# Kernel optimization log

Measured on AMD Instinct MI355X. Metric: run time of the kernel, lower is better.

The kernel has to match this reference:

```python
import jax, jax.numpy as jnp
import numpy as np

# ---- config constants (from configs) ----
B, L, C = 32, 512, 16
DM, DS, DCONV, EXP, EL = 128, 16, 4, 2, 2
PATCH, STRIDE, PAD, PRED = 16, 8, 8, 96
DIN = EXP * DM            # 256
DTR = (DM + 15) // 16     # dt_rank = 8
NPATCH = (L + 2 * PAD - PATCH) // STRIDE + 1   # 65
HNF = DM * NPATCH         # 8320
EPS = 1e-5


def setup_inputs() -> dict:
    key = jax.random.key(0)
    ks = jax.random.split(key, 14)
    n = jax.random.normal
    A_log = jnp.tile(jnp.log(jnp.arange(1, DS + 1, dtype=jnp.float32)), (EL, DIN, 1))
    return {
        "x_enc": n(ks[0], (B, L, C), jnp.float32),
        "x_mark_enc": n(ks[1], (B, L, 4), jnp.float32),
        "pe_w": n(ks[2], (DM, 1, PATCH), jnp.float32) * (1.0 / np.sqrt(PATCH)),
        "pe_b": n(ks[3], (DM,), jnp.float32) * 0.02,
        "in_proj_w": n(ks[4], (EL, 2 * DIN, DM), jnp.float32) * (1.0 / np.sqrt(DM)),
        "conv_w": n(ks[5], (EL, DIN, DCONV), jnp.float32) * (1.0 / np.sqrt(DCONV)),
        "conv_b": n(ks[6], (EL, DIN), jnp.float32) * 0.02,
        "x_proj_w": n(ks[7], (EL, DTR + 2 * DS, DIN), jnp.float32) * (1.0 / np.sqrt(DIN)),
        "dt_proj_w": n(ks[8], (EL, DIN, DTR), jnp.float32) * (1.0 / np.sqrt(DTR)),
        "dt_proj_b": n(ks[9], (EL, DIN), jnp.float32) * 0.1,
        "A_log": A_log,
        "D": jnp.ones((EL, DIN), jnp.float32),
        "out_proj_w": n(ks[10], (EL, DM, DIN), jnp.float32) * (1.0 / np.sqrt(DIN)),
        "head_w": n(ks[11], (PRED, HNF), jnp.float32) * (1.0 / np.sqrt(HNF)),
    }


def _silu(x):
    return x * jax.nn.sigmoid(x)


def _mamba(x, in_w, cw, cb, xp_w, dtp_w, dtp_b, A_log, Dp, out_w):
    # x: (b, P, DM)
    b = x.shape[0]
    xz = jnp.einsum('bpd,ed->bpe', x, in_w)            # (b, P, 2*DIN)
    xin, z = jnp.split(xz, 2, axis=-1)
    # causal depthwise conv1d over time
    xt = xin.transpose(0, 2, 1)                        # (b, DIN, P)
    conv = jax.lax.conv_general_dilated(
        xt, cw[:, None, :], (1,), [(DCONV - 1, 0)],
        dimension_numbers=('NCH', 'OIH', 'NCH'), feature_group_count=DIN)
    xc = _silu((conv + cb[None, :, None]).transpose(0, 2, 1))   # (b, P, DIN)
    dbc = jnp.einsum('bpd,ed->bpe', xc, xp_w)          # (b, P, DTR+2*DS)
    dt, Bm, Cm = jnp.split(dbc, [DTR, DTR + DS], axis=-1)
    dt = jax.nn.softplus(jnp.einsum('bpr,dr->bpd', dt, dtp_w) + dtp_b)  # (b,P,DIN)
    A = -jnp.exp(A_log)                                # (DIN, DS)

    def step(h, inp):
        dt_t, B_t, C_t, x_t = inp                      # (b,DIN),(b,DS),(b,DS),(b,DIN)
        dA = jnp.exp(dt_t[:, :, None] * A)             # (b,DIN,DS)
        h = dA * h + (dt_t * x_t)[:, :, None] * B_t[:, None, :]
        y = jnp.einsum('bds,bs->bd', h, C_t)
        return h, y

    h0 = jnp.zeros((b, DIN, DS), x.dtype)
    xs = (dt.transpose(1, 0, 2), Bm.transpose(1, 0, 2),
          Cm.transpose(1, 0, 2), xc.transpose(1, 0, 2))
    _, ys = jax.lax.scan(step, h0, xs)                 # (P, b, DIN)
    y = ys.transpose(1, 0, 2) + xc * Dp
    y = y * _silu(z)
    return jnp.einsum('bpd,od->bpo', y, out_w)         # (b, P, DM)


def reference(x_enc, x_mark_enc, pe_w, pe_b, in_proj_w, conv_w, conv_b,
              x_proj_w, dt_proj_w, dt_proj_b, A_log, D, out_proj_w, head_w):
    # RevIN-style normalization (stats detached, as in torch)
    mean = jax.lax.stop_gradient(jnp.mean(x_enc, axis=1, keepdims=True))
    xc = x_enc - mean
    std = jax.lax.stop_gradient(jnp.sqrt(jnp.var(xc, axis=1, keepdims=True) + EPS))
    xn = xc / std                                      # (B, L, C)
    x = xn.transpose(0, 2, 1).reshape(B * C, 1, L)
    # patch embedding conv
    p = jax.lax.conv_general_dilated(
        x, pe_w, (STRIDE,), [(PAD, PAD)],
        dimension_numbers=('NCH', 'OIH', 'NCH')) + pe_b[None, :, None]
    p = p.transpose(0, 2, 1)                           # (B*C, NPATCH, DM)
    for i in range(EL):
        p = _mamba(p, in_proj_w[i], conv_w[i], conv_b[i], x_proj_w[i],
                   dt_proj_w[i], dt_proj_b[i], A_log[i], D[i], out_proj_w[i])
    flat = p.reshape(B * C, HNF)
    head = flat @ head_w.T                             # (B*C, PRED)
    out = head.reshape(B, C, PRED).transpose(0, 2, 1)  # (B, PRED, C)
    return out * std + mean
```

## Files before the change

### kernel.cpp

```cpp
#include <hip/hip_runtime.h>

typedef __attribute__((ext_vector_type(8))) short bf16x8;
typedef __attribute__((ext_vector_type(8))) unsigned short u16x8;
typedef __attribute__((ext_vector_type(4))) float f32x4;

#define DEV static __device__ __forceinline__

constexpr int DM   = 128;
constexpr int DIN  = 256;
constexpr int NP   = 65;
constexpr int NSEQ = 512;
constexpr int HNF  = 8320;
constexpr int LOPL = NSEQ*HNF;

constexpr size_t OFF_FLAG = 0;
constexpr size_t OFF_MEAN = 16;
constexpr size_t OFF_STD  = OFF_MEAN + 512;
constexpr size_t OFF_ANEG = OFF_STD  + 512;
constexpr size_t OFF_CONVW= OFF_ANEG + 8192;
constexpr size_t OFF_CONVB= OFF_CONVW+ 2048;
constexpr size_t OFF_DTPB = OFF_CONVB+ 512;
constexpr size_t OFF_DD   = OFF_DTPB + 512;
constexpr size_t OFF_PEWT = OFF_DD   + 512;
constexpr size_t OFF_PEB  = OFF_PEWT + 2048;
constexpr size_t OFF_INF  = OFF_PEB  + 128;
constexpr size_t OFF_XPF  = OFF_INF  + 65536;
constexpr size_t OFF_OPF  = OFF_XPF  + 12288;
constexpr size_t OFF_HDF  = OFF_OPF  + 32768;
constexpr size_t OFF_PA   = OFF_HDF  + 399360;
constexpr size_t OFF_PB   = OFF_PA   + (size_t)NSEQ*HNF;
constexpr size_t OFF_HACC = OFF_PB;

DEV float b2f(unsigned short u){ union{unsigned v; float f;} x; x.v = ((unsigned)u)<<16; return x.f; }
DEV unsigned short f2b(float f){
  union{float f32; unsigned u;} x; x.f32 = f;
  unsigned r = x.u + 0x7fffu + ((x.u>>16)&1u);
  return (unsigned short)(r>>16);
}
DEV void split2(float v, unsigned short& h, unsigned short& l){
  h = f2b(v); l = f2b(v - b2f(h));
}
DEV float load_in(const void* p, size_t i, int isbf){
  return isbf ? b2f(((const unsigned short*)p)[i]) : ((const float*)p)[i];
}
DEV f32x4 mfma16(bf16x8 a, bf16x8 b, f32x4 c){
  return __builtin_amdgcn_mfma_f32_16x16x32_bf16(a,b,c,0,0,0);
}
constexpr float LOG2E = 1.4426950408889634f;
constexpr float LN2   = 0.6931471805599453f;
DEV float ex2(float x){ float r; asm("v_exp_f32 %0, %1" : "=v"(r) : "v"(x)); return r; }
DEV float lg2(float x){ float r; asm("v_log_f32 %0, %1" : "=v"(r) : "v"(x)); return r; }
DEV float frcp(float x){ float r; asm("v_rcp_f32 %0, %1" : "=v"(r) : "v"(x)); return r; }
DEV float sigm(float x){ return frcp(1.f + ex2(-x*LOG2E)); }
DEV float softplus(float x){
  float t = ex2(-fabsf(x)*LOG2E);
  return fmaxf(x,0.f) + LN2*lg2(1.f + t);
}
DEV int detect_bf16_wave(const void* x, int tid){
  const unsigned short* u = (const unsigned short*)x;
  unsigned short v = u[2*tid];
  int e = (v>>7)&0xff;
  int pred = (v==0) || (e>=100 && e<=141);
  unsigned long long m = __ballot(pred);
  return __popcll(m) >= 48;
}
DEV u16x8 load8_cvt(const void* p, size_t off, int isbf){
  u16x8 o;
  if (isbf){
    o = *(const u16x8*)((const unsigned short*)p + off);
  } else {
    const float* s = (const float*)p + off;
    float4 a = *(const float4*)(s), b = *(const float4*)(s+4);
    o[0]=f2b(a.x); o[1]=f2b(a.y); o[2]=f2b(a.z); o[3]=f2b(a.w);
    o[4]=f2b(b.x); o[5]=f2b(b.y); o[6]=f2b(b.z); o[7]=f2b(b.w);
  }
  return o;
}

constexpr size_t N_SMALL = 13952;
constexpr size_t N_IN8 = 16384, N_XP8 = 3072, N_OP8 = 8192, N_HD8 = 99840;
constexpr size_t N_BIG8 = N_IN8+N_XP8+N_OP8+N_HD8;
constexpr int NPREP = (int)((N_SMALL + N_BIG8 + 255)/256);
__global__ void k_pre(const void* x_enc, const void* pe_w, const void* pe_b,
                      const void* in_w, const void* conv_w, const void* conv_b,
                      const void* xp_w, const void* dtp_b,
                      const void* A_log, const void* Dm, const void* op_w,
                      const void* head_w, float* __restrict__ ws)
{
  const int tid = threadIdx.x;
  __shared__ int sflag;
  __shared__ float sx[512];
  __shared__ float spe[16*128];
  __shared__ float spb[128];
  __shared__ float rs[8], rq[8], sm[2];

  if (tid < 64){
    int f = detect_bf16_wave(x_enc, tid);
    if (tid==0) sflag = f;
  }
  __syncthreads();
  const int isbf = sflag;

  if (blockIdx.x < NPREP){
    if (blockIdx.x==0 && tid==0) ws[OFF_FLAG] = (float)isbf;
    size_t i = (size_t)blockIdx.x*256 + tid;
    const size_t nA=8192, nCW=2048, nCB=512, nDB=512, nD=512, nPW=2048, nPB=128;
    if (i < N_SMALL){
      if (i < nA){ ws[OFF_ANEG+i] = -__expf(load_in(A_log,i,isbf)); return; } i -= nA;
      if (i < nCW){ ws[OFF_CONVW+i] = load_in(conv_w,i,isbf); return; } i -= nCW;
      if (i < nCB){ ws[OFF_CONVB+i] = load_in(conv_b,i,isbf); return; } i -= nCB;
      if (i < nDB){ ws[OFF_DTPB+i]  = load_in(dtp_b,i,isbf); return; } i -= nDB;
      if (i < nD){  ws[OFF_DD+i]    = load_in(Dm,i,isbf); return; } i -= nD;
      if (i < nPW){ size_t k=i>>7, dm=i&127; ws[OFF_PEWT+i]=load_in(pe_w, dm*16+k, isbf); return; } i -= nPW;
      ws[OFF_PEB+i] = load_in(pe_b,i,isbf); return;
    }
    size_t i8 = i - N_SMALL;
    if (i8 >= N_BIG8) return;
    if (i8 < N_IN8){
      size_t lane=i8&63, kk=(i8>>6)&3, nt=(i8>>8)&31, l=i8>>13;
      size_t e=nt*16+(lane&15), k0=kk*32+((lane>>4)*8);
      ((u16x8*)((unsigned short*)(ws+OFF_INF)))[i8] =
        load8_cvt(in_w, (l*512+e)*128 + k0, isbf);
      return;
    } i8 -= N_IN8;
    if (i8 < N_XP8){
      size_t lane=i8&63, kk=(i8>>6)&7; size_t rest=i8>>9;
      size_t nt=rest%3, l=rest/3;
      size_t o=nt*16+(lane&15), k0=kk*32+((lane>>4)*8);
      u16x8 v;
      if (o<40) v = load8_cvt(xp_w, (l*40+o)*256 + k0, isbf);
      else { u16x8 z = {0,0,0,0,0,0,0,0}; v = z; }
      ((u16x8*)((unsigned short*)(ws+OFF_XPF)))[i8] = v;
      return;
    } i8 -= N_XP8;
    if (i8 < N_OP8){
      size_t lane=i8&63, kk=(i8>>6)&7, nt=(i8>>9)&7, l=i8>>12;
      size_t dm=nt*16+(lane&15), k0=kk*32+((lane>>4)*8);
      ((u16x8*)((unsigned short*)(ws+OFF_OPF)))[i8] =
        load8_cvt(op_w, (l*128+dm)*256 + k0, isbf);
      return;
    } i8 -= N_OP8;
    {
      size_t lane=i8&63, t=i8>>6;
      size_t kk=t%260, nt=t/260;
      size_t pr=nt*16+(lane&15), k0=kk*32+((lane>>4)*8);
      ((u16x8*)((unsigned short*)(ws+OFF_HDF)))[i8] =
        load8_cvt(head_w, pr*8320 + k0, isbf);
      return;
    }
  }

  const int n = blockIdx.x - NPREP;
  const int b = n>>4, c = n&15;

  float v0 = load_in(x_enc, ((size_t)b*512+tid)*16 + c, isbf);
  float v1 = load_in(x_enc, ((size_t)b*512+tid+256)*16 + c, isbf);
  float s = v0+v1, q = v0*v0+v1*v1;
  for (int o=32;o;o>>=1){ s += __shfl_down(s,o,64); q += __shfl_down(q,o,64); }
  const int w = tid>>6, lane = tid&63;
  if (lane==0){ rs[w]=s; rq[w]=q; }
  __syncthreads();
  if (tid==0){
    float S=rs[0]+rs[1]+rs[2]+rs[3], Q=rq[0]+rq[1]+rq[2]+rq[3];
    float mean = S*(1.f/512.f);
    float var = fmaxf(Q*(1.f/512.f)-mean*mean, 0.f);
    float sd = sqrtf(var+1e-5f);
    sm[0]=mean; sm[1]=1.f/sd;
    ws[OFF_MEAN+n]=mean; ws[OFF_STD+n]=sd;
  }
  __syncthreads();
  const float mean=sm[0], rstd=sm[1];
  sx[tid]=(v0-mean)*rstd; sx[tid+256]=(v1-mean)*rstd;
  for (int i=tid;i<2048;i+=256) spe[i]=load_in(pe_w, (size_t)(i&127)*16 + (i>>7), isbf);
  if (tid<128) spb[tid]=load_in(pe_b, tid, isbf);
  __syncthreads();

  unsigned short* pa_hi = (unsigned short*)(ws+OFF_PA);
  unsigned short* pa_lo = pa_hi + LOPL;
  for (int i=tid;i<NP*DM;i+=256){
    int t=i>>7, dm=i&127;
    float acc = spb[dm];
    int j0 = t*8-8;
    #pragma unroll
    for (int k=0;k<16;k++){ int j=j0+k; if ((unsigned)j<512u) acc += sx[j]*spe[k*128+dm]; }
    unsigned short h,lo2; split2(acc,h,lo2);
    pa_hi[(size_t)n*HNF+i] = h;
    pa_lo[(size_t)n*HNF+i] = lo2;
  }
}

__global__ __launch_bounds__(256,2)
void k_layer(int l, const unsigned short* __restrict__ pin,
             unsigned short* __restrict__ pout, float* __restrict__ ws,
             const void* __restrict__ dtp_w_raw)
{
  const int n = blockIdx.x, tid = threadIdx.x;
  const int w = tid>>6, lane = tid&63, ml = lane&15, quad = lane>>4;
  const int isbf = ws[OFF_FLAG] != 0.f;

  __shared__ __align__(16) unsigned char arena[79040];
  unsigned short* s_hi = (unsigned short*)arena;
  unsigned short* s_lo = (unsigned short*)(arena+34320);
  float* s_dbc = (float*)(arena+68640);

  const unsigned short* INF = (const unsigned short*)(ws+OFF_INF) + (size_t)l*65536;
  const unsigned short* XPF = (const unsigned short*)(ws+OFF_XPF) + (size_t)l*12288;
  const unsigned short* OPF = (const unsigned short*)(ws+OFF_OPF) + (size_t)l*32768;
  const unsigned short* phi = pin + (size_t)n*HNF;
  const unsigned short* plo = phi + LOPL;

  for (int pass=0; pass<2; ++pass){
    f32x4 acc[5][2];
    #pragma unroll
    for (int mt=0;mt<5;mt++){
      #pragma unroll
      for (int p2=0;p2<2;p2++){ f32x4 z={0.f,0.f,0.f,0.f}; acc[mt][p2]=z; }
    }
    bf16x8 ah[2][5], al[2][5];
    #pragma unroll
    for (int mt=0;mt<5;mt++){
      int row = mt*16+ml; if (row>64) row=64;
      ah[0][mt] = *(const bf16x8*)&phi[(size_t)row*128 + quad*8];
      al[0][mt] = *(const bf16x8*)&plo[(size_t)row*128 + quad*8];
    }
    #pragma unroll
    for (int kk=0;kk<4;kk++){
      const int cur = kk&1, nxt = cur^1;
      bf16x8 b0 = *(const bf16x8*)&INF[((size_t)((pass*8+w*2+0)*4+kk))*512 + lane*8];
      bf16x8 b1 = *(const bf16x8*)&INF[((size_t)((pass*8+w*2+1)*4+kk))*512 + lane*8];
      if (kk<3){
        #pragma unroll
        for (int mt=0;mt<5;mt++){
          int row = mt*16+ml; if (row>64) row=64;
          ah[nxt][mt] = *(const bf16x8*)&phi[(size_t)row*128 + (kk+1)*32 + quad*8];
          al[nxt][mt] = *(const bf16x8*)&plo[(size_t)row*128 + (kk+1)*32 + quad*8];
        }
      }
      #pragma unroll
      for (int mt=0;mt<5;mt++)
        acc[mt][0] = mfma16(ah[cur][mt],b0,mfma16(al[cur][mt],b0,acc[mt][0]));
      #pragma unroll
      for (int mt=0;mt<5;mt++)
        acc[mt][1] = mfma16(ah[cur][mt],b1,mfma16(al[cur][mt],b1,acc[mt][1]));
    }
    #pragma unroll
    for (int p2=0;p2<2;p2++){
      int e = (pass*8 + w*2 + p2)*16 + ml;
      #pragma unroll
      for (int mt=0;mt<5;mt++){
        #pragma unroll
        for (int r=0;r<4;r++){
          int t = mt*16+quad*4+r;
          if (t<NP){
            unsigned short h,lo2; split2(acc[mt][p2][r],h,lo2);
            s_hi[t*264+e]=h; s_lo[t*264+e]=lo2;
          }
        }
      }
    }
  }
  __syncthreads();

  {
    const int d = tid;
    const float4 wv = ((const float4*)(ws+OFF_CONVW))[l*256+d];
    const float bb = ws[OFF_CONVB + l*256+d];
    float x0=0.f,x1=0.f,x2=0.f;
    int t = 0;
    for (; t+4<=NP; t+=4){
      float xi0 = b2f(s_hi[(t+0)*264+d]) + b2f(s_lo[(t+0)*264+d]);
      float xi1 = b2f(s_hi[(t+1)*264+d]) + b2f(s_lo[(t+1)*264+d]);
      float xi2 = b2f(s_hi[(t+2)*264+d]) + b2f(s_lo[(t+2)*264+d]);
      float xi3 = b2f(s_hi[(t+3)*264+d]) + b2f(s_lo[(t+3)*264+d]);
      float v0 = bb + wv.x*x0  + wv.y*x1  + wv.z*x2  + wv.w*xi0;
      float v1 = bb + wv.x*x1  + wv.y*x2  + wv.z*xi0 + wv.w*xi1;
      float v2 = bb + wv.x*x2  + wv.y*xi0 + wv.z*xi1 + wv.w*xi2;
      float v3 = bb + wv.x*xi0 + wv.y*xi1 + wv.z*xi2 + wv.w*xi3;
      x0=xi1; x1=xi2; x2=xi3;
      float s0 = v0*sigm(v0), s1 = v1*sigm(v1), s2 = v2*sigm(v2), s3 = v3*sigm(v3);
      unsigned short h,lo2;
      split2(s0,h,lo2); s_hi[(t+0)*264+d]=h; s_lo[(t+0)*264+d]=lo2;
      split2(s1,h,lo2); s_hi[(t+1)*264+d]=h; s_lo[(t+1)*264+d]=lo2;
      split2(s2,h,lo2); s_hi[(t+2)*264+d]=h; s_lo[(t+2)*264+d]=lo2;
      split2(s3,h,lo2); s_hi[(t+3)*264+d]=h; s_lo[(t+3)*264+d]=lo2;
    }
    for (; t<NP; ++t){
      float xi = b2f(s_hi[t*264+d]) + b2f(s_lo[t*264+d]);
      float v = bb + wv.x*x0 + wv.y*x1 + wv.z*x2 + wv.w*xi;
      x0=x1; x1=x2; x2=xi;
      float sv = v * sigm(v);
      unsigned short h,lo2; split2(sv,h,lo2);
      s_hi[t*264+d]=h; s_lo[t*264+d]=lo2;
    }
  }
  __syncthreads();

  for (int tile=w; tile<15; tile+=4){
    int mt=tile/3, nt=tile%3;
    f32x4 acc={0.f,0.f,0.f,0.f};
    #pragma unroll
    for (int kk=0;kk<8;kk++){
      int row = mt*16+ml; if (row>64) row=64;
      bf16x8 ah = *(const bf16x8*)&s_hi[row*264 + kk*32 + quad*8];
      bf16x8 al = *(const bf16x8*)&s_lo[row*264 + kk*32 + quad*8];
      bf16x8 b  = *(const bf16x8*)&XPF[((size_t)(nt*8+kk))*512 + lane*8];
      acc = mfma16(ah,b,mfma16(al,b,acc));
    }
    int o = nt*16+ml;
    #pragma unroll
    for (int r=0;r<4;r++){
      int t=mt*16+quad*4+r;
      if (t<NP && o<40) s_dbc[t*40+o] = acc[r];
    }
  }
  __syncthreads();

  {
    const int d = tid;
    float A2[16];
    {
      const float4* ap = (const float4*)(ws+OFF_ANEG) + ((size_t)l*256+d)*4;
      #pragma unroll
      for (int qq=0;qq<4;qq++){
        float4 t4 = ap[qq];
        A2[qq*4]=t4.x*LOG2E; A2[qq*4+1]=t4.y*LOG2E; A2[qq*4+2]=t4.z*LOG2E; A2[qq*4+3]=t4.w*LOG2E;
      }
    }
    int fastbit = 1;
    #pragma unroll
    for (int ss=0;ss<16;ss++){
      float ex = -(float)(ss+1)*LOG2E;
      fastbit &= (fabsf(A2[ss]-ex) <= 1e-4f*(float)(ss+1)) ? 1 : 0;
    }
    const int fastu = __all(fastbit);
    const float Dv = ws[OFF_DD + l*256+d];
    const float bias = ws[OFF_DTPB + l*256+d];
    float wdt[8];
    #pragma unroll
    for (int r=0;r<8;r++) wdt[r] = load_in(dtp_w_raw, ((size_t)l*256+d)*8+r, isbf);
    float h[16];
    #pragma unroll
    for (int ss=0;ss<16;ss++) h[ss]=0.f;

    float4 q0 = *(const float4*)&s_dbc[0];
    float4 q1 = *(const float4*)&s_dbc[4];
    float xh = b2f(s_hi[d]), xl = b2f(s_lo[d]);

    for (int t=0;t<NP;t++){
      const float* row = &s_dbc[t*40];
      float xv = xh + xl;
      float4 b0=*(const float4*)(row+8),  b1=*(const float4*)(row+12),
             b2v=*(const float4*)(row+16), b3=*(const float4*)(row+20);
      float4 c0=*(const float4*)(row+24), c1=*(const float4*)(row+28),
             c2=*(const float4*)(row+32), c3=*(const float4*)(row+36);
      float4 nq0, nq1; float nxh=0.f, nxl=0.f;
      if (t+1<NP){
        const float* nrow = &s_dbc[(t+1)*40];
        nq0 = *(const float4*)(nrow);
        nq1 = *(const float4*)(nrow+4);
        nxh = b2f(s_hi[(t+1)*264+d]); nxl = b2f(s_lo[(t+1)*264+d]);
      }
      float p0 = q0.x*wdt[0] + q0.y*wdt[1];
      float p1 = q0.z*wdt[2] + q0.w*wdt[3];
      float p2 = q1.x*wdt[4] + q1.y*wdt[5];
      float p3 = q1.z*wdt[6] + q1.w*wdt[7];
      float din = (bias + p0 + p1) + (p2 + p3);
      float dtv = softplus(din);
      float dtx = dtv*xv;
      float Bv[16], Cv[16];
      Bv[0]=b0.x;Bv[1]=b0.y;Bv[2]=b0.z;Bv[3]=b0.w; Bv[4]=b1.x;Bv[5]=b1.y;Bv[6]=b1.z;Bv[7]=b1.w;
      Bv[8]=b2v.x;Bv[9]=b2v.y;Bv[10]=b2v.z;Bv[11]=b2v.w; Bv[12]=b3.x;Bv[13]=b3.y;Bv[14]=b3.z;Bv[15]=b3.w;
      Cv[0]=c0.x;Cv[1]=c0.y;Cv[2]=c0.z;Cv[3]=c0.w; Cv[4]=c1.x;Cv[5]=c1.y;Cv[6]=c1.z;Cv[7]=c1.w;
      Cv[8]=c2.x;Cv[9]=c2.y;Cv[10]=c2.z;Cv[11]=c2.w; Cv[12]=c3.x;Cv[13]=c3.y;Cv[14]=c3.z;Cv[15]=c3.w;
      float rr[16];
      if (fastu){
        float r1 = ex2(-dtv*LOG2E);
        float r2=r1*r1;
        float r3=r2*r1, r4=r2*r2;
        float r5=r4*r1, r6=r4*r2, r7=r4*r3, r8=r4*r4;
        rr[0]=r1; rr[1]=r2; rr[2]=r3; rr[3]=r4;
        rr[4]=r5; rr[5]=r6; rr[6]=r7; rr[7]=r8;
        rr[8]=r8*r1; rr[9]=r8*r2; rr[10]=r8*r3; rr[11]=r8*r4;
        rr[12]=r8*r5; rr[13]=r8*r6; rr[14]=r8*r7; rr[15]=r8*r8;
      } else {
        #pragma unroll
        for (int ss=0;ss<16;ss++) rr[ss] = ex2(dtv*A2[ss]);
      }
      float y0 = 0.f, y1 = 0.f;
      #pragma unroll
      for (int ss=0;ss<16;ss+=2){
        h[ss]   = rr[ss]*h[ss]     + dtx*Bv[ss];
        h[ss+1] = rr[ss+1]*h[ss+1] + dtx*Bv[ss+1];
        y0 += h[ss]*Cv[ss];
        y1 += h[ss+1]*Cv[ss+1];
      }
      float g0 = (y0+y1) + xv*Dv;
      unsigned short hh,lo2; split2(g0,hh,lo2);
      s_hi[t*264+d]=hh; s_lo[t*264+d]=lo2;
      q0=nq0; q1=nq1; xh=nxh; xl=nxl;
    }
  }
  __syncthreads();

  {
    bf16x8 ah[2][4], al[2][4];
    {
      int row = ml;
      #pragma unroll
      for (int kk=0;kk<4;kk++){
        ah[0][kk] = *(const bf16x8*)&phi[(size_t)row*128 + kk*32 + quad*8];
        al[0][kk] = *(const bf16x8*)&plo[(size_t)row*128 + kk*32 + quad*8];
      }
    }
    #pragma unroll
    for (int mt=0; mt<5; ++mt){
      const int cur = mt&1, nxt = cur^1;
      if (mt<4){
        int row = (mt+1)*16+ml; if (row>64) row=64;
        #pragma unroll
        for (int kk=0;kk<4;kk++){
          ah[nxt][kk] = *(const bf16x8*)&phi[(size_t)row*128 + kk*32 + quad*8];
          al[nxt][kk] = *(const bf16x8*)&plo[(size_t)row*128 + kk*32 + quad*8];
        }
      }
      #pragma unroll
      for (int j=0;j<4;j++){
        int nt = w + j*4;
        f32x4 acc={0.f,0.f,0.f,0.f};
        #pragma unroll
        for (int kk=0;kk<4;kk++){
          bf16x8 b = *(const bf16x8*)&INF[((size_t)((16+nt)*4+kk))*512 + lane*8];
          acc = mfma16(ah[cur][kk],b,mfma16(al[cur][kk],b,acc));
        }
        int d = nt*16+ml;
        #pragma unroll
        for (int r=0;r<4;r++){
          int t = mt*16+quad*4+r;
          if (t<NP){
            float g0 = b2f(s_hi[t*264+d]) + b2f(s_lo[t*264+d]);
            float zv = acc[r];
            float g = g0 * zv * sigm(zv);
            unsigned short hh,lo2; split2(g,hh,lo2);
            s_hi[t*264+d]=hh; s_lo[t*264+d]=lo2;
          }
        }
      }
    }
  }
  __syncthreads();

  {
    f32x4 acc[5][2];
    #pragma unroll
    for (int mt=0;mt<5;mt++){
      #pragma unroll
      for (int p2=0;p2<2;p2++){ f32x4 z={0.f,0.f,0.f,0.f}; acc[mt][p2]=z; }
    }
    bf16x8 bpre[2][2];
    bpre[0][0] = *(const bf16x8*)&OPF[((size_t)((w*2+0)*8+0))*512 + lane*8];
    bpre[0][1] = *(const bf16x8*)&OPF[((size_t)((w*2+1)*8+0))*512 + lane*8];
    #pragma unroll
    for (int kk=0;kk<8;kk++){
      const int cur = kk&1, nxt = cur^1;
      if (kk<7){
        bpre[nxt][0] = *(const bf16x8*)&OPF[((size_t)((w*2+0)*8+kk+1))*512 + lane*8];
        bpre[nxt][1] = *(const bf16x8*)&OPF[((size_t)((w*2+1)*8+kk+1))*512 + lane*8];
      }
      bf16x8 ah[5], al[5];
      #pragma unroll
      for (int mt=0;mt<5;mt++){
        int row = mt*16+ml; if (row>64) row=64;
        ah[mt] = *(const bf16x8*)&s_hi[row*264 + kk*32 + quad*8];
        al[mt] = *(const bf16x8*)&s_lo[row*264 + kk*32 + quad*8];
      }
      #pragma unroll
      for (int mt=0;mt<5;mt++)
        acc[mt][0] = mfma16(ah[mt],bpre[cur][0],mfma16(al[mt],bpre[cur][0],acc[mt][0]));
      #pragma unroll
      for (int mt=0;mt<5;mt++)
        acc[mt][1] = mfma16(ah[mt],bpre[cur][1],mfma16(al[mt],bpre[cur][1],acc[mt][1]));
    }
    #pragma unroll
    for (int p2=0;p2<2;p2++){
      int dm = (w*2+p2)*16+ml;
      #pragma unroll
      for (int mt=0;mt<5;mt++){
        #pragma unroll
        for (int r=0;r<4;r++){
          int t = mt*16+quad*4+r;
          if (t<NP){
            unsigned short hh,lo2; split2(acc[mt][p2][r],hh,lo2);
            pout[(size_t)n*HNF + t*128 + dm] = hh;
            pout[(size_t)n*HNF + t*128 + dm + LOPL] = lo2;
          }
        }
      }
    }
  }
}

__global__ __launch_bounds__(512,2)
void k_headp(const float* __restrict__ ws, float* __restrict__ hacc)
{
  const int blk = blockIdx.x;
  const int p = blk & 7, mt = blk >> 3;
  const int tid = threadIdx.x, w = tid>>6, lane = tid&63, ml = lane&15, quad = lane>>4;
  const int base  = (p<4) ? p*33 : 132 + (p-4)*32;
  const int count = (p<4) ? 33 : 32;
  const unsigned short* pa_hi = (const unsigned short*)(ws+OFF_PA);
  const unsigned short* pa_lo = pa_hi + LOPL;
  const unsigned short* HDF = (const unsigned short*)(ws+OFF_HDF);
  __shared__ float red[8][64][4];

  f32x4 acc[6];
  #pragma unroll
  for (int nt=0;nt<6;nt++){ f32x4 z={0.f,0.f,0.f,0.f}; acc[nt]=z; }

  const size_t abase = (size_t)(mt*16+ml)*HNF + quad*8;
  for (int i=w; i<count; i+=8){
    const int kk = base + i;
    bf16x8 ah = *(const bf16x8*)(pa_hi + abase + (size_t)kk*32);
    bf16x8 al = *(const bf16x8*)(pa_lo + abase + (size_t)kk*32);
    #pragma unroll
    for (int nt=0;nt<6;nt++){
      bf16x8 b = *(const bf16x8*)&HDF[((size_t)(nt*260+kk))*512 + lane*8];
      acc[nt] = mfma16(ah,b,mfma16(al,b,acc[nt]));
    }
  }

  for (int nt=0;nt<6;nt++){
    #pragma unroll
    for (int r=0;r<4;r++) red[w][lane][r] = acc[nt][r];
    __syncthreads();
    if (w==0){
      #pragma unroll
      for (int r=0;r<4;r++){
        float s = red[0][lane][r]+red[1][lane][r]+red[2][lane][r]+red[3][lane][r]
                + red[4][lane][r]+red[5][lane][r]+red[6][lane][r]+red[7][lane][r];
        hacc[((size_t)(mt*6+nt)*8 + p)*256 + lane*4 + r] = s;
      }
    }
    __syncthreads();
  }
}

__global__ void k_fin(const float* __restrict__ ws, void* __restrict__ out)
{
  const int tile = blockIdx.x;
  const int nt = tile%6, mt = tile/6;
  const int lane = threadIdx.x, ml = lane&15, quad = lane>>4;
  const float* hacc = ws + OFF_HACC;
  const int isbf = ws[OFF_FLAG]!=0.f;
  #pragma unroll
  for (int r=0;r<4;r++){
    size_t base = (size_t)tile*8*256 + lane*4 + r;
    float s = 0.f;
    #pragma unroll
    for (int p=0;p<8;p++) s += hacc[base + (size_t)p*256];
    int nseq = mt*16 + quad*4 + r;
    int pred = nt*16 + ml;
    float val = s*ws[OFF_STD+nseq] + ws[OFF_MEAN+nseq];
    size_t o = ((size_t)(nseq>>4)*96 + pred)*16 + (nseq&15);
    if (isbf) ((unsigned short*)out)[o] = f2b(val);
    else      ((float*)out)[o] = val;
  }
}

extern "C" void kernel_launch(void* const* d_in, const int* in_sizes, int n_in,
                              void* d_out, int out_size, void* d_ws, size_t ws_size,
                              hipStream_t stream)
{
  (void)in_sizes; (void)n_in; (void)out_size; (void)ws_size;
  float* ws = (float*)d_ws;
  const void* x_enc = d_in[0];
  const void* pe_w  = d_in[2];  const void* pe_b  = d_in[3];
  const void* in_w  = d_in[4];  const void* conv_w= d_in[5];
  const void* conv_b= d_in[6];  const void* xp_w  = d_in[7];
  const void* dtp_w = d_in[8];  const void* dtp_b = d_in[9];
  const void* A_log = d_in[10]; const void* Dm    = d_in[11];
  const void* op_w  = d_in[12]; const void* head_w= d_in[13];

  k_pre<<<NPREP+NSEQ,256,0,stream>>>(x_enc,pe_w,pe_b,in_w,conv_w,conv_b,xp_w,
                                     dtp_b,A_log,Dm,op_w,head_w,ws);
  unsigned short* pa = (unsigned short*)(ws+OFF_PA);
  unsigned short* pb = (unsigned short*)(ws+OFF_PB);
  k_layer<<<NSEQ,256,0,stream>>>(0,pa,pb,ws,dtp_w);
  k_layer<<<NSEQ,256,0,stream>>>(1,pb,pa,ws,dtp_w);
  k_headp<<<256,512,0,stream>>>(ws, ws+OFF_HACC);
  k_fin<<<192,64,0,stream>>>(ws, d_out);
}
```

Measured before the change: 254.3 us.

## Fuse causal depthwise conv and SiLU into in-proj MFMA epilogue via lane shuffles

The separate pass that reread the in-projection output from shared memory, ran the 4-tap causal conv plus SiLU, and wrote it back is removed. The conv is now computed directly on the MFMA accumulators, with the three previous timesteps fetched from neighbouring lanes or the previous M-tile through cross-lane shuffles. This saves a shared-memory round trip, one barrier and the hi/lo bf16 split/rejoin of the intermediate, at the cost of extra shuffles and more register pressure in the epilogue. The conv input is now the exact fp32 accumulator rather than the split bf16 pair.

```diff
diff --git a/kernel.cpp b/kernel.cpp
--- a/kernel.cpp
+++ b/kernel.cpp
@@ -243,54 +243,38 @@
       for (int mt=0;mt<5;mt++)
         acc[mt][1] = mfma16(ah[cur][mt],b1,mfma16(al[cur][mt],b1,acc[mt][1]));
     }
+    const int psrc = (lane+48)&63;
     #pragma unroll
     for (int p2=0;p2<2;p2++){
-      int e = (pass*8 + w*2 + p2)*16 + ml;
+      const int e = (pass*8 + w*2 + p2)*16 + ml;
+      const float4 wv = ((const float4*)(ws+OFF_CONVW))[l*256+e];
+      const float bb = ws[OFF_CONVB + l*256+e];
       #pragma unroll
       for (int mt=0;mt<5;mt++){
-        #pragma unroll
-        for (int r=0;r<4;r++){
-          int t = mt*16+quad*4+r;
-          if (t<NP){
-            unsigned short h,lo2; split2(acc[mt][p2][r],h,lo2);
-            s_hi[t*264+e]=h; s_lo[t*264+e]=lo2;
-          }
+        const float a0=acc[mt][p2][0], a1=acc[mt][p2][1],
+                    a2=acc[mt][p2][2], a3=acc[mt][p2][3];
+        float c1=__shfl(a1,psrc,64), c2=__shfl(a2,psrc,64), c3=__shfl(a3,psrc,64);
+        float pm1=0.f, pm2=0.f, pm3=0.f;
+        if (mt>0){
+          pm1=__shfl(acc[mt-1][p2][1],psrc,64);
+          pm2=__shfl(acc[mt-1][p2][2],psrc,64);
+          pm3=__shfl(acc[mt-1][p2][3],psrc,64);
         }
-      }
-    }
-  }
-  __syncthreads();
-
-  {
-    const int d = tid;
-    const float4 wv = ((const float4*)(ws+OFF_CONVW))[l*256+d];
-    const float bb = ws[OFF_CONVB + l*256+d];
-    float x0=0.f,x1=0.f,x2=0.f;
-    int t = 0;
-    for (; t+4<=NP; t+=4){
-      float xi0 = b2f(s_hi[(t+0)*264+d]) + b2f(s_lo[(t+0)*264+d]);
-      float xi1 = b2f(s_hi[(t+1)*264+d]) + b2f(s_lo[(t+1)*264+d]);
-      float xi2 = b2f(s_hi[(t+2)*264+d]) + b2f(s_lo[(t+2)*264+d]);
-      float xi3 = b2f(s_hi[(t+3)*264+d]) + b2f(s_lo[(t+3)*264+d]);
-      float v0 = bb + wv.x*x0  + wv.y*x1  + wv.z*x2  + wv.w*xi0;
-      float v1 = bb + wv.x*x1  + wv.y*x2  + wv.z*xi0 + wv.w*xi1;
-      float v2 = bb + wv.x*x2  + wv.y*xi0 + wv.z*xi1 + wv.w*xi2;
-      float v3 = bb + wv.x*xi0 + wv.y*xi1 + wv.z*xi2 + wv.w*xi3;
-      x0=xi1; x1=xi2; x2=xi3;
-      float s0 = v0*sigm(v0), s1 = v1*sigm(v1), s2 = v2*sigm(v2), s3 = v3*sigm(v3);
-      unsigned short h,lo2;
-      split2(s0,h,lo2); s_hi[(t+0)*264+d]=h; s_lo[(t+0)*264+d]=lo2;
-      split2(s1,h,lo2); s_hi[(t+1)*264+d]=h; s_lo[(t+1)*264+d]=lo2;
-      split2(s2,h,lo2); s_hi[(t+2)*264+d]=h; s_lo[(t+2)*264+d]=lo2;
-      split2(s3,h,lo2); s_hi[(t+3)*264+d]=h; s_lo[(t+3)*264+d]=lo2;
-    }
-    for (; t<NP; ++t){
-      float xi = b2f(s_hi[t*264+d]) + b2f(s_lo[t*264+d]);
-      float v = bb + wv.x*x0 + wv.y*x1 + wv.z*x2 + wv.w*xi;
-      x0=x1; x1=x2; x2=xi;
-      float sv = v * sigm(v);
-      unsigned short h,lo2; split2(sv,h,lo2);
-      s_hi[t*264+d]=h; s_lo[t*264+d]=lo2;
+        const float xm1 = (quad==0)? pm1 : c1;
+        const float xm2 = (quad==0)? pm2 : c2;
+        const float xm3 = (quad==0)? pm3 : c3;
+        float v0 = bb + wv.x*xm1 + wv.y*xm2 + wv.z*xm3 + wv.w*a0;
+        float v1 = bb + wv.x*xm2 + wv.y*xm3 + wv.z*a0  + wv.w*a1;
+        float v2 = bb + wv.x*xm3 + wv.y*a0  + wv.z*a1  + wv.w*a2;
+        float v3 = bb + wv.x*a0  + wv.y*a1  + wv.z*a2  + wv.w*a3;
+        float s0=v0*sigm(v0), s1=v1*sigm(v1), s2=v2*sigm(v2), s3=v3*sigm(v3);
+        const int tb = mt*16 + quad*4;
+        unsigned short hh,lo2;
+        if (tb+0<NP){ split2(s0,hh,lo2); s_hi[(tb+0)*264+e]=hh; s_lo[(tb+0)*264+e]=lo2; }
+        if (tb+1<NP){ split2(s1,hh,lo2); s_hi[(tb+1)*264+e]=hh; s_lo[(tb+1)*264+e]=lo2; }
+        if (tb+2<NP){ split2(s2,hh,lo2); s_hi[(tb+2)*264+e]=hh; s_lo[(tb+2)*264+e]=lo2; }
+        if (tb+3<NP){ split2(s3,hh,lo2); s_hi[(tb+3)*264+e]=hh; s_lo[(tb+3)*264+e]=lo2; }
+      }
     }
   }
   __syncthreads();
```

New measurement: 256.9 us. About the same (+1.0%).
